# Kernel tuning notes

Measured on AMD Instinct MI355X. Metric: run time of the kernel, lower is better.

Reference implementation:

```python
import jax, jax.numpy as jnp
import numpy as np

# sizes
A, P, E = 2000, 20000, 200000
MUL0, MUL1 = 128, 64            # 128x0e + 64x1o
DIM = MUL0 + 3 * MUL1            # 320
NBASIS, FC_HID = 10, 100
WNUM = MUL0 + MUL0 + MUL1 + MUL1 # 384 tp weights per edge
MID0 = MUL0 + MUL1               # 192 scalar channels in irreps_mid
NUM_NEIGHBORS = 10.0


def setup_inputs() -> dict:
    key = jax.random.key(0)
    ks = jax.random.split(key, 20)
    # edge attr = spherical harmonics lmax=1 (component norm): [1, sqrt(3)*unit_vec]
    vec = jax.random.normal(ks[0], (E, 3))
    unit = vec / jnp.linalg.norm(vec, axis=1, keepdims=True)
    edge_attr = jnp.concatenate([jnp.ones((E, 1)), jnp.sqrt(3.0) * unit], axis=1)
    return {
        "sender_input": jax.random.normal(ks[1], (A, DIM)),
        "sender_attr": jnp.ones((A, 1)),
        "receiver_input": jax.random.normal(ks[2], (P, DIM)),
        "receiver_attr": jnp.ones((P, 1)),
        "edge_src": jax.random.randint(ks[3], (E,), 0, A, dtype=jnp.int32),
        "edge_dst": jax.random.randint(ks[4], (E,), 0, P, dtype=jnp.int32),
        "edge_attr": edge_attr,
        "edge_scalars": jax.random.normal(ks[5], (E, NBASIS)),  # normalized radial basis
        # FC net (no bias, e3nn FullyConnectedNet style)
        "fc_w1": jax.random.normal(ks[6], (NBASIS, FC_HID)),
        "fc_w2": jax.random.normal(ks[7], (FC_HID, WNUM)),
        # lin1: FCTP(sender, 0e, sender) -> per-l linear on multiplicities
        "lin1_w0": jax.random.normal(ks[8], (MUL0, MUL0)),
        "lin1_w1": jax.random.normal(ks[9], (MUL1, MUL1)),
        # sc: FCTP(receiver, 0e, output)
        "sc_w0": jax.random.normal(ks[10], (MUL0, MUL0)),
        "sc_w1": jax.random.normal(ks[11], (MUL1, MUL1)),
        # lin2: FCTP(mid, 0e, output)
        "lin2_w0": jax.random.normal(ks[12], (MID0, MUL0)),
        "lin2_w1": jax.random.normal(ks[13], (MID0, MUL1)),
        # lin3: FCTP(mid, 0e, 0e) -> only scalar part contributes
        "lin3_w": jax.random.normal(ks[14], (MID0, 1)),
    }


def reference(sender_input, sender_attr, receiver_input, receiver_attr,
              edge_src, edge_dst, edge_attr, edge_scalars,
              fc_w1, fc_w2, lin1_w0, lin1_w1, sc_w0, sc_w1,
              lin2_w0, lin2_w1, lin3_w):
    f32 = jnp.float32
    # per-edge tensor-product weights from radial MLP (silu, fan-in normalized)
    h = jax.nn.silu(edge_scalars @ fc_w1 * (1.0 / np.sqrt(NBASIS)))
    weight = h @ fc_w2 * (1.0 / np.sqrt(FC_HID))                      # [E, 384]

    # self-connection on receivers (scalar attr -> per-l linear)
    r_in = receiver_input * receiver_attr
    sc0 = r_in[:, :MUL0] @ sc_w0 * (1.0 / np.sqrt(MUL0))              # [P,128]
    sc1 = jnp.einsum('pum,uv->pvm', r_in[:, MUL0:].reshape(-1, MUL1, 3), sc_w1) * (1.0 / np.sqrt(MUL1))
    sc_out = jnp.concatenate([sc0, sc1.reshape(-1, 3 * MUL1)], axis=1)  # [P,320]

    # lin1 on senders
    s_in = sender_input * sender_attr
    s0 = s_in[:, :MUL0] @ lin1_w0 * (1.0 / np.sqrt(MUL0))             # [A,128]
    s1 = jnp.einsum('aum,uv->avm', s_in[:, MUL0:].reshape(-1, MUL1, 3), lin1_w1) * (1.0 / np.sqrt(MUL1))

    # gather sender features to edges
    g0 = s0[edge_src]                                                  # [E,128]
    g1 = s1[edge_src]                                                  # [E,64,3]
    sh0 = edge_attr[:, :1]                                             # [E,1]
    sh1 = edge_attr[:, 1:]                                             # [E,3]

    # weighted 'uvu' tensor product paths (instruction order)
    w0 = weight[:, :MUL0]
    w1 = weight[:, MUL0:2 * MUL0]
    w2 = weight[:, 2 * MUL0:2 * MUL0 + MUL1]
    w3 = weight[:, 2 * MUL0 + MUL1:]
    out0a = w0 * g0 * sh0                                              # 0e x 0e -> 0e  [E,128]
    out1a = (w1 * g0)[:, :, None] * sh1[:, None, :]                    # 0e x 1o -> 1o  [E,128,3]
    out1b = w2[:, :, None] * g1 * sh0[:, None, :]                      # 1o x 0e -> 1o  [E,64,3]
    out0b = w3 * jnp.einsum('eum,em->eu', g1, sh1) * (1.0 / np.sqrt(3.0))  # 1o x 1o -> 0e [E,64]
    # irreps_mid sorted: 128x0e + 64x0e + 128x1o + 64x1o  -> 768 dims
    edge_feat = jnp.concatenate([out0a, out0b,
                                 out1a.reshape(-1, 3 * MUL0),
                                 out1b.reshape(-1, 3 * MUL1)], axis=1)

    # scatter-add to receivers
    r = jax.ops.segment_sum(edge_feat, edge_dst, num_segments=receiver_input.shape[0])
    r = r * (1.0 / np.sqrt(NUM_NEIGHBORS))                             # [P,768]
    r = r * receiver_attr
    r0 = r[:, :MID0]
    r1 = r[:, MID0:].reshape(-1, MID0, 3)

    conv0 = r0 @ lin2_w0 * (1.0 / np.sqrt(MID0))                        # [P,128]
    conv1 = jnp.einsum('pum,uv->pvm', r1, lin2_w1) * (1.0 / np.sqrt(MID0))
    conv_out = jnp.concatenate([conv0, conv1.reshape(-1, 3 * MUL1)], axis=1)

    angle = 0.1 * (r0 @ lin3_w * (1.0 / np.sqrt(MID0)))                 # [P,1]
    # sc.output_mask is all-ones here (every output irrep has a path)
    return jnp.cos(angle) * sc_out + jnp.sin(angle) * conv_out          # [P,320]
```

## Files before the change

kernel.cpp:

```cpp
#include <hip/hip_runtime.h>
#include <hip/hip_bf16.h>
#include <math.h>

#define A_N    2000
#define P_N    20000
#define PPAD   20032
#define E_N    200000
#define MUL0   128
#define MUL1   64
#define DIM    320
#define NBASIS 10
#define FC_HID 100
#define WNUM   384
#define MID0   192
#define OV     128
#define SSTRIDE 392

#define RS10   0.31622776601683794f
#define RS100  0.1f
#define RS128  0.08838834764831845f
#define RS64   0.125f
#define RS192  0.07216878364870323f
#define RS3    0.5773502691896258f
#define RSNEI  0.31622776601683794f

typedef __bf16 bf16x8 __attribute__((ext_vector_type(8)));
typedef float  f32x4  __attribute__((ext_vector_type(4)));

__device__ __forceinline__ float bflo(unsigned u) { return __uint_as_float(u << 16); }
__device__ __forceinline__ float bfhi(unsigned u) { return __uint_as_float(u & 0xffff0000u); }

__global__ __launch_bounds__(320) void sender_kernel(
    const float* __restrict__ sender_input, const float* __restrict__ sender_attr,
    const float* __restrict__ lin1_w0, const float* __restrict__ lin1_w1,
    __bf16* __restrict__ s_pack)
{
    __shared__ float sin_s[DIM];
    const int a = blockIdx.x;
    const int t = threadIdx.x;
    const float attr = sender_attr[a];
    sin_s[t] = sender_input[(size_t)a * DIM + t] * attr;
    __syncthreads();
    __bf16* row = s_pack + (size_t)a * 384;
    if (t < MUL0) {
        float acc = 0.f;
        for (int u = 0; u < MUL0; ++u)
            acc = fmaf(sin_s[u], lin1_w0[u * MUL0 + t], acc);
        row[(t & 63) * 6 + (t >> 6)] = (__bf16)(acc * RS128);
    } else {
        const int idx = t - MUL0;
        const int v = idx / 3, m = idx - 3 * v;
        float acc = 0.f;
        for (int u = 0; u < MUL1; ++u)
            acc = fmaf(sin_s[MUL0 + 3 * u + m], lin1_w1[u * MUL1 + v], acc);
        row[v * 6 + 2 + m] = (__bf16)(acc * RS64);
    }
    if (t < 64) row[t * 6 + 5] = (__bf16)0.f;
}

__global__ __launch_bounds__(256) void hist_kernel(
    const int* __restrict__ edge_dst, int* __restrict__ counts)
{
    const int e = blockIdx.x * 256 + threadIdx.x;
    if (e < E_N) atomicAdd(&counts[edge_dst[e]], 1);
}

__global__ __launch_bounds__(1024) void scan_kernel(
    const int* __restrict__ counts, int* __restrict__ head)
{
    __shared__ int part[1024];
    const int t = threadIdx.x;
    const int base = t * 20;
    int c[20];
    int s = 0;
    #pragma unroll
    for (int i = 0; i < 20; ++i) {
        const int p = base + i;
        c[i] = (p < P_N) ? counts[p] : 0;
        s += c[i];
    }
    part[t] = s;
    __syncthreads();
    for (int off = 1; off < 1024; off <<= 1) {
        const int v = (t >= off) ? part[t - off] : 0;
        __syncthreads();
        part[t] += v;
        __syncthreads();
    }
    int run = (t > 0) ? part[t - 1] : 0;
    #pragma unroll
    for (int i = 0; i < 20; ++i) {
        const int p = base + i;
        if (p < P_N) { head[p] = run; run += c[i]; }
    }
}

__global__ __launch_bounds__(256) void scatter_kernel(
    const int* __restrict__ edge_dst, const int* __restrict__ edge_src,
    const float4* __restrict__ edge_attr4,
    int* __restrict__ head, int* __restrict__ sorted,
    int* __restrict__ src_sorted, float4* __restrict__ attr_sorted)
{
    const int e = blockIdx.x * 256 + threadIdx.x;
    if (e < E_N) {
        const int pos = atomicAdd(&head[edge_dst[e]], 1);
        sorted[pos]      = e;
        src_sorted[pos]  = edge_src[e];
        attr_sorted[pos] = edge_attr4[e];
    }
}

__global__ __launch_bounds__(256) void pack_w2_kernel(
    const float* __restrict__ fc_w2, __bf16* __restrict__ w2p)
{
    const int tid  = blockIdx.x * 256 + threadIdx.x;
    const int lane = tid & 63;
    const int g    = (tid >> 6) & 3;
    const int n    = tid >> 8;
    const int col  = n * 16 + (lane & 15);
    const int kb   = g * 32 + 8 * (lane >> 4);
    bf16x8 v;
    #pragma unroll
    for (int i = 0; i < 8; ++i) {
        const int k = kb + i;
        v[i] = (__bf16)((k < FC_HID) ? fc_w2[k * WNUM + col] * RS100 : 0.f);
    }
    ((bf16x8*)w2p)[tid] = v;
}

__global__ __launch_bounds__(256) void pack_kernel(
    const float* __restrict__ src, __bf16* __restrict__ dst,
    int K, int KG, int N, float scale)
{
    const int tid  = blockIdx.x * 256 + threadIdx.x;
    const int lane = tid & 63;
    const int fi   = tid >> 6;
    const int g    = fi % KG;
    const int n    = fi / KG;
    const int col  = n * 16 + (lane & 15);
    const int kb   = g * 32 + 8 * (lane >> 4);
    bf16x8 v;
    #pragma unroll
    for (int i = 0; i < 8; ++i) {
        const int k = kb + i;
        v[i] = (__bf16)((k < K) ? src[(size_t)k * N + col] * scale : 0.f);
    }
    ((bf16x8*)dst)[tid] = v;
}

__global__ __launch_bounds__(256) void mlp_gemm_chunk_kernel(
    const int* __restrict__ sorted,
    const float* __restrict__ edge_scalars,
    const float* __restrict__ fc_w1, const __bf16* __restrict__ w2p,
    __bf16* __restrict__ wbuf, int cLo)
{
    __shared__ float  fc1s[NBASIS * 128];
    __shared__ float  es_s[64][11];
    __shared__ __attribute__((aligned(16))) __bf16 hstage[32 * SSTRIDE];

    const int tid   = threadIdx.x;
    const int wave  = tid >> 6;
    const int lane  = tid & 63;
    const int pbase = blockIdx.x * 64;

    for (int f = tid; f < 64 * NBASIS; f += 256) {
        const int e = f / NBASIS, i = f - e * NBASIS;
        int gi = cLo + pbase + e;
        if (gi >= E_N) gi = E_N - 1;
        es_s[e][i] = edge_scalars[(size_t)sorted[gi] * NBASIS + i];
    }
    for (int f = tid; f < NBASIS * FC_HID; f += 256) {
        const int i = f / FC_HID, k = f - i * FC_HID;
        fc1s[i * 128 + (k ^ ((k & 96) >> 3))] = fc_w1[f];
    }
    __syncthreads();

    __bf16* h_lds = hstage;
    {
        const int e  = tid >> 2;
        const int k0 = (tid & 3) * 32;
        const int kx = (tid & 3) * 4;
        float es[NBASIS];
        #pragma unroll
        for (int i = 0; i < NBASIS; ++i) es[i] = es_s[e][i];
        #pragma unroll
        for (int o = 0; o < 4; ++o) {
            bf16x8 hv;
            #pragma unroll
            for (int j = 0; j < 8; ++j) {
                const int r = o * 8 + j;
                const int k = k0 + r;
                float x = 0.f;
                if (k < FC_HID) {
                    const int ks = k0 + (r ^ kx);
                    #pragma unroll
                    for (int i = 0; i < NBASIS; ++i)
                        x = fmaf(es[i], fc1s[i * 128 + ks], x);
                    x *= RS10;
                    x = x / (1.f + __expf(-x));
                }
                hv[j] = (__bf16)x;
            }
            const int idx = (e * 128 + k0 + o * 8) ^ ((e & 7) << 3);
            *(bf16x8*)&h_lds[idx] = hv;
        }
    }
    __syncthreads();

    bf16x8 a[4][4];
    const int arow = lane & 15, ag = lane >> 4;
    #pragma unroll
    for (int mt = 0; mt < 4; ++mt) {
        const int e = mt * 16 + arow;
        #pragma unroll
        for (int g = 0; g < 4; ++g) {
            const int idx = (e * 128 + g * 32 + ag * 8) ^ ((e & 7) << 3);
            a[mt][g] = *(const bf16x8*)&h_lds[idx];
        }
    }

    const bf16x8* w2v = (const bf16x8*)w2p;
    const int row0 = 4 * (lane >> 4), col16 = lane & 15;

    #pragma unroll
    for (int half = 0; half < 2; ++half) {
        __syncthreads();
        #pragma unroll 2
        for (int nt = 0; nt < 6; ++nt) {
            const int ntile = wave * 6 + nt;
            bf16x8 b[4];
            #pragma unroll
            for (int g = 0; g < 4; ++g)
                b[g] = w2v[(ntile * 4 + g) * 64 + lane];
            const int L = ntile * 16 + col16;
            const int slot = (L & 63) * 6 + (L >> 6);
            #pragma unroll
            for (int mtl = 0; mtl < 2; ++mtl) {
                const int mt = half * 2 + mtl;
                f32x4 acc = {0.f, 0.f, 0.f, 0.f};
                #pragma unroll
                for (int g = 0; g < 4; ++g)
                    acc = __builtin_amdgcn_mfma_f32_16x16x32_bf16(a[mt][g], b[g],
                                                                  acc, 0, 0, 0);
                __bf16* sp = &hstage[(mtl * 16 + row0) * SSTRIDE + slot];
                #pragma unroll
                for (int j = 0; j < 4; ++j)
                    sp[j * SSTRIDE] = (__bf16)acc[j];
            }
        }
        __syncthreads();
        const int srow = tid >> 3;
        const float4* sp4 = (const float4*)&hstage[srow * SSTRIDE + (tid & 7) * 48];
        float4* gp4 = (float4*)((char*)wbuf
                      + (size_t)(pbase + half * 32 + srow) * 768
                      + (size_t)(tid & 7) * 96);
        #pragma unroll
        for (int q = 0; q < 6; ++q) gp4[q] = sp4[q];
    }
}

__global__ __launch_bounds__(256) void gather_kernel(
    const int* __restrict__ head, const int* __restrict__ counts,
    const int* __restrict__ src_sorted, const float4* __restrict__ attr_sorted,
    const __bf16* __restrict__ wbuf, const __bf16* __restrict__ s_pack,
    const float* __restrict__ receiver_input, const float* __restrict__ receiver_attr,
    const float* __restrict__ lin3_w,
    __bf16* __restrict__ rbuf, __bf16* __restrict__ rinp,
    float* __restrict__ cs_arr, float* __restrict__ sn_arr,
    int cLo, int cHi)
{
    __shared__ int sel_s[4];
    const int tid  = threadIdx.x;
    const int wave = tid >> 6;
    const int lane = tid & 63;
    const int p = blockIdx.x * 4 + wave;

    const int cnt   = counts[p];
    const int start = head[p] - cnt;
    const int sel   = (start >= cLo) & (start < cHi);

    if (lane == 0) sel_s[wave] = sel;
    __syncthreads();
    if ((sel_s[0] | sel_s[1] | sel_s[2] | sel_s[3]) == 0) return;
    if (!sel) return;

    float acc[12];
    #pragma unroll
    for (int i = 0; i < 12; ++i) acc[i] = 0.f;

    if (cnt > 0) {
        const char* wb  = (const char*)wbuf;
        const char* spk = (const char*)s_pack;
        const int last = start + cnt - 1;

        const unsigned* wq0 = (const unsigned*)(wb + (size_t)(start - cLo) * 768 + lane * 12);
        unsigned cw0 = wq0[0], cw1 = wq0[1], cw2 = wq0[2];
        float4 cea = attr_sorted[start];
        int csrc = src_sorted[start];
        const unsigned* sq0 = (const unsigned*)(spk + (size_t)csrc * 768 + lane * 12);
        unsigned cs0 = sq0[0], cs1 = sq0[1], cs2 = sq0[2];
        int nsrc = src_sorted[(start + 1 <= last) ? start + 1 : last];

        for (int i = 0; i < cnt; ++i) {
            const int pn = (start + i + 1 <= last) ? start + i + 1 : last;
            const unsigned* wqn = (const unsigned*)(wb + (size_t)(pn - cLo) * 768 + lane * 12);
            const unsigned nw0 = wqn[0], nw1 = wqn[1], nw2 = wqn[2];
            const float4 nea = attr_sorted[pn];
            const unsigned* sqn = (const unsigned*)(spk + (size_t)nsrc * 768 + lane * 12);
            const unsigned ns0 = sqn[0], ns1 = sqn[1], ns2 = sqn[2];
            int p2 = start + i + 2; if (p2 > last) p2 = last;
            const int nnsrc = src_sorted[p2];

            const float sh0 = cea.x, sh1x = cea.y, sh1y = cea.z, sh1z = cea.w;
            const float w0a = bflo(cw0), w0b = bfhi(cw0);
            const float w1a = bflo(cw1), w1b = bfhi(cw1);
            const float w2v = bflo(cw2), w3v = bfhi(cw2);
            const float g0a = bflo(cs0), g0b = bfhi(cs0);
            const float g1x = bflo(cs1), g1y = bfhi(cs1), g1z = bflo(cs2);

            acc[0] = fmaf(w0a * g0a, sh0, acc[0]);
            acc[1] = fmaf(w0b * g0b, sh0, acc[1]);
            const float dotg = fmaf(g1x, sh1x, fmaf(g1y, sh1y, g1z * sh1z)) * RS3;
            acc[2] = fmaf(w3v, dotg, acc[2]);
            const float p1a = w1a * g0a, p1b = w1b * g0b;
            acc[3] = fmaf(p1a, sh1x, acc[3]);
            acc[4] = fmaf(p1a, sh1y, acc[4]);
            acc[5] = fmaf(p1a, sh1z, acc[5]);
            acc[6] = fmaf(p1b, sh1x, acc[6]);
            acc[7] = fmaf(p1b, sh1y, acc[7]);
            acc[8] = fmaf(p1b, sh1z, acc[8]);
            const float q = w2v * sh0;
            acc[9]  = fmaf(q, g1x, acc[9]);
            acc[10] = fmaf(q, g1y, acc[10]);
            acc[11] = fmaf(q, g1z, acc[11]);

            cw0 = nw0; cw1 = nw1; cw2 = nw2;
            cs0 = ns0; cs1 = ns1; cs2 = ns2;
            cea = nea; nsrc = nnsrc;
        }
    }

    const float rattr = receiver_attr[p];
    const float rfac  = RSNEI * rattr;
    const float v0 = acc[0] * rfac, v1 = acc[1] * rfac, v2 = acc[2] * rfac;

    float part = v0 * lin3_w[lane] + v1 * lin3_w[64 + lane] + v2 * lin3_w[128 + lane];
    #pragma unroll
    for (int off = 1; off < 64; off <<= 1) part += __shfl_xor(part, off);
    if (lane == 0) {
        const float a = part * 0.1f * RS192;
        cs_arr[p] = __cosf(a);
        sn_arr[p] = __sinf(a);
    }

    __bf16* rb = rbuf + (size_t)p * 768;
    rb[lane]       = (__bf16)v0;
    rb[64 + lane]  = (__bf16)v1;
    rb[128 + lane] = (__bf16)v2;
    #pragma unroll
    for (int m = 0; m < 3; ++m) {
        __bf16* r1 = rb + 192 + m * 192;
        r1[lane]        = (__bf16)(acc[3 + m] * rfac);
        r1[64 + lane]   = (__bf16)(acc[6 + m] * rfac);
        r1[128 + lane]  = (__bf16)(acc[9 + m] * rfac);
    }

    __bf16* rp = rinp + (size_t)p * 320;
    #pragma unroll
    for (int q = 0; q < 5; ++q) {
        const int t = q * 64 + lane;
        const float val = receiver_input[(size_t)p * DIM + t] * rattr;
        int pos;
        if (t < 128) pos = t;
        else { const int idx = t - 128; const int u = idx / 3, m = idx - 3 * u;
               pos = 128 + m * 64 + u; }
        rp[pos] = (__bf16)val;
    }
}

__global__ __launch_bounds__(256) void out_transform_kernel(
    const __bf16* __restrict__ rbuf, const __bf16* __restrict__ rinp,
    const __bf16* __restrict__ scw0p, const __bf16* __restrict__ l2w0p,
    const __bf16* __restrict__ scw1p, const __bf16* __restrict__ l2w1p,
    const float* __restrict__ cs_arr, const float* __restrict__ sn_arr,
    float* __restrict__ out, int nbS)
{
    const int wave = threadIdx.x >> 6, lane = threadIdx.x & 63;
    const bool vec = (int)blockIdx.x >= nbS;
    const int b = vec ? (int)blockIdx.x - nbS : (int)blockIdx.x;
    const int pw0 = b * 64 + wave * 16;
    const int arow = lane & 15, ag = lane >> 4;
    const int crow0 = 4 * (lane >> 4), ccol = lane & 15;

    const size_t riRow = (size_t)(pw0 + arow) * 320;
    const size_t rbRow = (size_t)(pw0 + arow) * 768;

    float cs[4], sn[4];
    #pragma unroll
    for (int j = 0; j < 4; ++j) {
        cs[j] = cs_arr[pw0 + crow0 + j];
        sn[j] = sn_arr[pw0 + crow0 + j];
    }

    if (!vec) {
        bf16x8 ain[4], arr[6];
        #pragma unroll
        for (int g = 0; g < 4; ++g)
            ain[g] = *(const bf16x8*)&rinp[riRow + g * 32 + ag * 8];
        #pragma unroll
        for (int g = 0; g < 6; ++g)
            arr[g] = *(const bf16x8*)&rbuf[rbRow + g * 32 + ag * 8];
        #pragma unroll
        for (int nt = 0; nt < 8; ++nt) {
            f32x4 asc = {0.f, 0.f, 0.f, 0.f}, acv = {0.f, 0.f, 0.f, 0.f};
            #pragma unroll
            for (int g = 0; g < 4; ++g)
                asc = __builtin_amdgcn_mfma_f32_16x16x32_bf16(
                    ain[g], ((const bf16x8*)scw0p)[(nt * 4 + g) * 64 + lane], asc, 0, 0, 0);
            #pragma unroll
            for (int g = 0; g < 6; ++g)
                acv = __builtin_amdgcn_mfma_f32_16x16x32_bf16(
                    arr[g], ((const bf16x8*)l2w0p)[(nt * 6 + g) * 64 + lane], acv, 0, 0, 0);
            #pragma unroll
            for (int j = 0; j < 4; ++j) {
                const int row = pw0 + crow0 + j;
                if (row < P_N)
                    out[(size_t)row * DIM + nt * 16 + ccol] =
                        cs[j] * asc[j] + sn[j] * acv[j];
            }
        }
    } else {
        #pragma unroll
        for (int m = 0; m < 3; ++m) {
            bf16x8 ain1[2], arr1[6];
            #pragma unroll
            for (int g = 0; g < 2; ++g)
                ain1[g] = *(const bf16x8*)&rinp[riRow + 128 + m * 64 + g * 32 + ag * 8];
            #pragma unroll
            for (int g = 0; g < 6; ++g)
                arr1[g] = *(const bf16x8*)&rbuf[rbRow + 192 + m * 192 + g * 32 + ag * 8];
            #pragma unroll
            for (int vt = 0; vt < 4; ++vt) {
                f32x4 asc = {0.f, 0.f, 0.f, 0.f}, acv = {0.f, 0.f, 0.f, 0.f};
                #pragma unroll
                for (int g = 0; g < 2; ++g)
                    asc = __builtin_amdgcn_mfma_f32_16x16x32_bf16(
                        ain1[g], ((const bf16x8*)scw1p)[(vt * 2 + g) * 64 + lane], asc, 0, 0, 0);
                #pragma unroll
                for (int g = 0; g < 6; ++g)
                    acv = __builtin_amdgcn_mfma_f32_16x16x32_bf16(
                        arr1[g], ((const bf16x8*)l2w1p)[(vt * 6 + g) * 64 + lane], acv, 0, 0, 0);
                #pragma unroll
                for (int j = 0; j < 4; ++j) {
                    const int row = pw0 + crow0 + j;
                    if (row < P_N) {
                        const int v = vt * 16 + ccol;
                        out[(size_t)row * DIM + MUL0 + 3 * v + m] =
                            cs[j] * asc[j] + sn[j] * acv[j];
                    }
                }
            }
        }
    }
}

extern "C" void kernel_launch(void* const* d_in, const int* in_sizes, int n_in,
                              void* d_out, int out_size, void* d_ws, size_t ws_size,
                              hipStream_t stream)
{
    const float* sender_input   = (const float*)d_in[0];
    const float* sender_attr    = (const float*)d_in[1];
    const float* receiver_input = (const float*)d_in[2];
    const float* receiver_attr  = (const float*)d_in[3];
    const int*   edge_src       = (const int*)  d_in[4];
    const int*   edge_dst       = (const int*)  d_in[5];
    const float* edge_attr      = (const float*)d_in[6];
    const float* edge_scalars   = (const float*)d_in[7];
    const float* fc_w1          = (const float*)d_in[8];
    const float* fc_w2          = (const float*)d_in[9];
    const float* lin1_w0        = (const float*)d_in[10];
    const float* lin1_w1        = (const float*)d_in[11];
    const float* sc_w0          = (const float*)d_in[12];
    const float* sc_w1          = (const float*)d_in[13];
    const float* lin2_w0        = (const float*)d_in[14];
    const float* lin2_w1        = (const float*)d_in[15];
    const float* lin3_w         = (const float*)d_in[16];
    float* out = (float*)d_out;

    char* wsb = (char*)d_ws;
    float4* attr_sorted = (float4*)wsb;
    __bf16* s_pack = (__bf16*)(wsb + (size_t)E_N * 16);
    __bf16* w2p    = s_pack + (size_t)A_N * 384;
    __bf16* scw0p  = w2p   + 24 * 4 * 64 * 8;
    __bf16* l2w0p  = scw0p +  8 * 4 * 64 * 8;
    __bf16* scw1p  = l2w0p +  8 * 6 * 64 * 8;
    __bf16* l2w1p  = scw1p +  4 * 2 * 64 * 8;
    __bf16* rbuf   = l2w1p +  4 * 6 * 64 * 8;
    __bf16* rinp   = rbuf + (size_t)PPAD * 768;
    float*  cs_arr = (float*)(rinp + (size_t)PPAD * 320);
    float*  sn_arr = cs_arr + PPAD;
    int* counts     = (int*)(sn_arr + PPAD);
    int* head       = counts + P_N;
    int* sorted     = head + P_N;
    int* src_sorted = sorted + E_N;
    __bf16* wbuf    = (__bf16*)(src_sorted + E_N);
    const size_t fixedB = (size_t)((char*)wbuf - wsb);

    long long maxpos = (long long)((ws_size - fixedB) / 768);
    long long cc = (maxpos - OV - 64) & ~63LL;
    int cchunk = (cc > E_N) ? E_N : (int)cc;

    sender_kernel<<<A_N, 320, 0, stream>>>(sender_input, sender_attr,
                                           lin1_w0, lin1_w1, s_pack);
    pack_w2_kernel<<<24, 256, 0, stream>>>(fc_w2, w2p);
    pack_kernel<<< 8, 256, 0, stream>>>(sc_w0,   scw0p, 128, 4, 128, RS128);
    pack_kernel<<<12, 256, 0, stream>>>(lin2_w0, l2w0p, 192, 6, 128, RS192);
    pack_kernel<<< 2, 256, 0, stream>>>(sc_w1,   scw1p, 64,  2, 64,  RS64);
    pack_kernel<<< 6, 256, 0, stream>>>(lin2_w1, l2w1p, 192, 6, 64,  RS192);

    hipMemsetAsync(counts, 0, P_N * sizeof(int), stream);
    hist_kernel<<<(E_N + 255) / 256, 256, 0, stream>>>(edge_dst, counts);
    scan_kernel<<<1, 1024, 0, stream>>>(counts, head);
    scatter_kernel<<<(E_N + 255) / 256, 256, 0, stream>>>(
        edge_dst, edge_src, (const float4*)edge_attr,
        head, sorted, src_sorted, attr_sorted);

    for (int cLo = 0; cLo < E_N; cLo += cchunk) {
        int nPos = E_N - cLo;
        if (nPos > cchunk + OV) nPos = cchunk + OV;
        const int cHi = (cLo + cchunk >= E_N) ? (E_N + 1) : (cLo + cchunk);
        mlp_gemm_chunk_kernel<<<(nPos + 63) / 64, 256, 0, stream>>>(
            sorted, edge_scalars, fc_w1, w2p, wbuf, cLo);
        gather_kernel<<<P_N / 4, 256, 0, stream>>>(
            head, counts, src_sorted, attr_sorted, wbuf, s_pack,
            receiver_input, receiver_attr, lin3_w,
            rbuf, rinp, cs_arr, sn_arr, cLo, cHi);
    }

    const int nbS = PPAD / 64;
    out_transform_kernel<<<2 * nbS, 256, 0, stream>>>(
        rbuf, rinp, scw0p, l2w0p, scw1p, l2w1p, cs_arr, sn_arr, out, nbS);
}
```

Baseline: 244.7 us.

## Compute MLP hidden in registers, store GEMM results directly, merge pack kernels

The radial MLP kernel now has each wave compute its own 16-edge A fragment straight into MFMA register layout. This removes the LDS staging of hidden activations and the LDS transpose buffer for outputs. Results go to global memory as packed bf16 pairs in the interleaved slot layout, with fewer barriers and less LDS. The five weight-packing launches are merged into one kernel to cut launch overhead. In exchange the global stores are 12-byte strided rather than coalesced float4, and the fc_w1 bank swizzle is dropped.

```diff
diff --git a/kernel.cpp b/kernel.cpp
--- a/kernel.cpp
+++ b/kernel.cpp
@@ -14,7 +14,6 @@
 #define WNUM   384
 #define MID0   192
 #define OV     128
-#define SSTRIDE 392
 
 #define RS10   0.31622776601683794f
 #define RS100  0.1f
@@ -29,6 +28,12 @@
 
 __device__ __forceinline__ float bflo(unsigned u) { return __uint_as_float(u << 16); }
 __device__ __forceinline__ float bfhi(unsigned u) { return __uint_as_float(u & 0xffff0000u); }
+__device__ __forceinline__ unsigned pkbf(float lo, float hi) {
+    __bf16 a = (__bf16)lo, b = (__bf16)hi;
+    unsigned short ua = __builtin_bit_cast(unsigned short, a);
+    unsigned short ub = __builtin_bit_cast(unsigned short, b);
+    return (unsigned)ua | ((unsigned)ub << 16);
+}
 
 __global__ __launch_bounds__(320) void sender_kernel(
     const float* __restrict__ sender_input, const float* __restrict__ sender_attr,
@@ -110,29 +115,10 @@
     }
 }
 
-__global__ __launch_bounds__(256) void pack_w2_kernel(
-    const float* __restrict__ fc_w2, __bf16* __restrict__ w2p)
-{
-    const int tid  = blockIdx.x * 256 + threadIdx.x;
-    const int lane = tid & 63;
-    const int g    = (tid >> 6) & 3;
-    const int n    = tid >> 8;
-    const int col  = n * 16 + (lane & 15);
-    const int kb   = g * 32 + 8 * (lane >> 4);
-    bf16x8 v;
-    #pragma unroll
-    for (int i = 0; i < 8; ++i) {
-        const int k = kb + i;
-        v[i] = (__bf16)((k < FC_HID) ? fc_w2[k * WNUM + col] * RS100 : 0.f);
-    }
-    ((bf16x8*)w2p)[tid] = v;
-}
-
-__global__ __launch_bounds__(256) void pack_kernel(
+__device__ __forceinline__ void pack_one(
     const float* __restrict__ src, __bf16* __restrict__ dst,
-    int K, int KG, int N, float scale)
-{
-    const int tid  = blockIdx.x * 256 + threadIdx.x;
+    int K, int KG, int N, float scale, int tid)
+{
     const int lane = tid & 63;
     const int fi   = tid >> 6;
     const int g    = fi % KG;
@@ -148,18 +134,32 @@
     ((bf16x8*)dst)[tid] = v;
 }
 
+__global__ __launch_bounds__(256) void pack_all_kernel(
+    const float* __restrict__ fc_w2,   __bf16* __restrict__ w2p,
+    const float* __restrict__ sc_w0,   __bf16* __restrict__ scw0p,
+    const float* __restrict__ lin2_w0, __bf16* __restrict__ l2w0p,
+    const float* __restrict__ sc_w1,   __bf16* __restrict__ scw1p,
+    const float* __restrict__ lin2_w1, __bf16* __restrict__ l2w1p)
+{
+    const int b = blockIdx.x;
+    if (b < 24)      pack_one(fc_w2,   w2p,   FC_HID, 4, WNUM, RS100, b * 256 + threadIdx.x);
+    else if (b < 32) pack_one(sc_w0,   scw0p, 128,    4, 128,  RS128, (b - 24) * 256 + threadIdx.x);
+    else if (b < 44) pack_one(lin2_w0, l2w0p, 192,    6, 128,  RS192, (b - 32) * 256 + threadIdx.x);
+    else if (b < 46) pack_one(sc_w1,   scw1p, 64,     2, 64,   RS64,  (b - 44) * 256 + threadIdx.x);
+    else             pack_one(lin2_w1, l2w1p, 192,    6, 64,   RS192, (b - 46) * 256 + threadIdx.x);
+}
+
 __global__ __launch_bounds__(256) void mlp_gemm_chunk_kernel(
     const int* __restrict__ sorted,
     const float* __restrict__ edge_scalars,
     const float* __restrict__ fc_w1, const __bf16* __restrict__ w2p,
     __bf16* __restrict__ wbuf, int cLo)
 {
-    __shared__ float  fc1s[NBASIS * 128];
-    __shared__ float  es_s[64][11];
-    __shared__ __attribute__((aligned(16))) __bf16 hstage[32 * SSTRIDE];
+    __shared__ float fc1s[NBASIS * 128];
+    __shared__ float es_s[64][11];
 
     const int tid   = threadIdx.x;
-    const int wave  = tid >> 6;
+    const int mt    = tid >> 6;
     const int lane  = tid & 63;
     const int pbase = blockIdx.x * 64;
 
@@ -171,91 +171,59 @@
     }
     for (int f = tid; f < NBASIS * FC_HID; f += 256) {
         const int i = f / FC_HID, k = f - i * FC_HID;
-        fc1s[i * 128 + (k ^ ((k & 96) >> 3))] = fc_w1[f];
+        fc1s[i * 128 + k] = fc_w1[f];
     }
     __syncthreads();
 
-    __bf16* h_lds = hstage;
-    {
-        const int e  = tid >> 2;
-        const int k0 = (tid & 3) * 32;
-        const int kx = (tid & 3) * 4;
-        float es[NBASIS];
-        #pragma unroll
-        for (int i = 0; i < NBASIS; ++i) es[i] = es_s[e][i];
-        #pragma unroll
-        for (int o = 0; o < 4; ++o) {
-            bf16x8 hv;
-            #pragma unroll
-            for (int j = 0; j < 8; ++j) {
-                const int r = o * 8 + j;
-                const int k = k0 + r;
-                float x = 0.f;
-                if (k < FC_HID) {
-                    const int ks = k0 + (r ^ kx);
-                    #pragma unroll
-                    for (int i = 0; i < NBASIS; ++i)
-                        x = fmaf(es[i], fc1s[i * 128 + ks], x);
-                    x *= RS10;
-                    x = x / (1.f + __expf(-x));
-                }
-                hv[j] = (__bf16)x;
+    const int r = lane & 15, q = lane >> 4;
+
+    float es[NBASIS];
+    #pragma unroll
+    for (int i = 0; i < NBASIS; ++i) es[i] = es_s[mt * 16 + r][i];
+
+    bf16x8 a[4];
+    #pragma unroll
+    for (int g = 0; g < 4; ++g) {
+        #pragma unroll
+        for (int i2 = 0; i2 < 8; ++i2) {
+            const int k = g * 32 + 8 * q + i2;
+            float x = 0.f;
+            if (k < FC_HID) {
+                #pragma unroll
+                for (int i = 0; i < NBASIS; ++i)
+                    x = fmaf(es[i], fc1s[i * 128 + k], x);
+                x *= RS10;
+                x = x / (1.f + __expf(-x));
             }
-            const int idx = (e * 128 + k0 + o * 8) ^ ((e & 7) << 3);
-            *(bf16x8*)&h_lds[idx] = hv;
+            a[g][i2] = (__bf16)x;
         }
     }
-    __syncthreads();
-
-    bf16x8 a[4][4];
-    const int arow = lane & 15, ag = lane >> 4;
-    #pragma unroll
-    for (int mt = 0; mt < 4; ++mt) {
-        const int e = mt * 16 + arow;
-        #pragma unroll
-        for (int g = 0; g < 4; ++g) {
-            const int idx = (e * 128 + g * 32 + ag * 8) ^ ((e & 7) << 3);
-            a[mt][g] = *(const bf16x8*)&h_lds[idx];
+
+    const bf16x8* w2v = (const bf16x8*)w2p;
+    const int rowB = pbase + mt * 16 + 4 * q;
+
+    #pragma unroll
+    for (int t = 0; t < 4; ++t) {
+        f32x4 wa[6];
+        #pragma unroll
+        for (int s = 0; s < 6; ++s) {
+            const int nt = 4 * s + t;
+            f32x4 acc = {0.f, 0.f, 0.f, 0.f};
+            #pragma unroll
+            for (int g = 0; g < 4; ++g)
+                acc = __builtin_amdgcn_mfma_f32_16x16x32_bf16(
+                    a[g], w2v[(nt * 4 + g) * 64 + lane], acc, 0, 0, 0);
+            wa[s] = acc;
         }
-    }
-
-    const bf16x8* w2v = (const bf16x8*)w2p;
-    const int row0 = 4 * (lane >> 4), col16 = lane & 15;
-
-    #pragma unroll
-    for (int half = 0; half < 2; ++half) {
-        __syncthreads();
-        #pragma unroll 2
-        for (int nt = 0; nt < 6; ++nt) {
-            const int ntile = wave * 6 + nt;
-            bf16x8 b[4];
-            #pragma unroll
-            for (int g = 0; g < 4; ++g)
-                b[g] = w2v[(ntile * 4 + g) * 64 + lane];
-            const int L = ntile * 16 + col16;
-            const int slot = (L & 63) * 6 + (L >> 6);
-            #pragma unroll
-            for (int mtl = 0; mtl < 2; ++mtl) {
-                const int mt = half * 2 + mtl;
-                f32x4 acc = {0.f, 0.f, 0.f, 0.f};
-                #pragma unroll
-                for (int g = 0; g < 4; ++g)
-                    acc = __builtin_amdgcn_mfma_f32_16x16x32_bf16(a[mt][g], b[g],
-                                                                  acc, 0, 0, 0);
-                __bf16* sp = &hstage[(mtl * 16 + row0) * SSTRIDE + slot];
-                #pragma unroll
-                for (int j = 0; j < 4; ++j)
-                    sp[j * SSTRIDE] = (__bf16)acc[j];
-            }
+        const int laneP = t * 16 + r;
+        #pragma unroll
+        for (int j = 0; j < 4; ++j) {
+            unsigned* dst = (unsigned*)((char*)wbuf
+                           + (size_t)(rowB + j) * 768 + laneP * 12);
+            dst[0] = pkbf(wa[0][j], wa[1][j]);
+            dst[1] = pkbf(wa[2][j], wa[3][j]);
+            dst[2] = pkbf(wa[4][j], wa[5][j]);
         }
-        __syncthreads();
-        const int srow = tid >> 3;
-        const float4* sp4 = (const float4*)&hstage[srow * SSTRIDE + (tid & 7) * 48];
-        float4* gp4 = (float4*)((char*)wbuf
-                      + (size_t)(pbase + half * 32 + srow) * 768
-                      + (size_t)(tid & 7) * 96);
-        #pragma unroll
-        for (int q = 0; q < 6; ++q) gp4[q] = sp4[q];
     }
 }
 
@@ -512,11 +480,9 @@
 
     sender_kernel<<<A_N, 320, 0, stream>>>(sender_input, sender_attr,
                                            lin1_w0, lin1_w1, s_pack);
-    pack_w2_kernel<<<24, 256, 0, stream>>>(fc_w2, w2p);
-    pack_kernel<<< 8, 256, 0, stream>>>(sc_w0,   scw0p, 128, 4, 128, RS128);
-    pack_kernel<<<12, 256, 0, stream>>>(lin2_w0, l2w0p, 192, 6, 128, RS192);
-    pack_kernel<<< 2, 256, 0, stream>>>(sc_w1,   scw1p, 64,  2, 64,  RS64);
-    pack_kernel<<< 6, 256, 0, stream>>>(lin2_w1, l2w1p, 192, 6, 64,  RS192);
+    pack_all_kernel<<<52, 256, 0, stream>>>(fc_w2, w2p, sc_w0, scw0p,
+                                            lin2_w0, l2w0p, sc_w1, scw1p,
+                                            lin2_w1, l2w1p);
 
     hipMemsetAsync(counts, 0, P_N * sizeof(int), stream);
     hist_kernel<<<(E_N + 255) / 256, 256, 0, stream>>>(edge_dst, counts);
```

Result: slower. 249.9 us (+2.1%).
